# Kernel tuning notes

Hardware: AMD Instinct MI355X
Metric: run time of the kernel (lower is better)

Reference implementation:

```python
import jax, jax.numpy as jnp
import numpy as np

TINY = 1e-9
S, V, H, W = 2, 4, 1024, 1024
PATCH, SKIP = 2, 2
C = PATCH * SKIP
PIX_PER_VIEW = 4096
NP_COARSE = PIX_PER_VIEW // (PATCH * PATCH)   # top-k on coarse grid
N_SAMPLED = NP_COARSE * PATCH * PATCH         # total fine pixels per view
ON_MASK = 0.9
AT_CENTER = 0.8
HC, WC = H // C, W // C


def setup_inputs() -> dict:
    key = jax.random.key(0)
    k1, k2, k3, k4, k5 = jax.random.split(key, 5)
    ys, xs = jnp.meshgrid(jnp.arange(H, dtype=jnp.float32),
                          jnp.arange(W, dtype=jnp.float32), indexing='ij')
    uv1 = jnp.stack([xs.reshape(-1), ys.reshape(-1)])            # (2, H*W): X then Y
    uv = jnp.broadcast_to(uv1[None, None], (S, V, 2, H * W)) + 0.0
    base = jnp.array([[1111.0, 0.0, W / 2.0, 0.0],
                      [0.0, 1111.0, H / 2.0, 0.0],
                      [0.0, 0.0, 1.0, 0.0],
                      [0.0, 0.0, 0.0, 1.0]], dtype=jnp.float32)
    intrinsics = jnp.broadcast_to(base[None], (S, 4, 4)) + 0.0
    A = jax.random.normal(k2, (S, V, 3, 3), dtype=jnp.float32)
    Q, _ = jnp.linalg.qr(A)                                       # random rotations
    t = 2.0 * jax.random.normal(k3, (S, V, 3), dtype=jnp.float32)
    ext = jnp.zeros((S, V, 4, 4), dtype=jnp.float32)
    ext = ext.at[..., :3, :3].set(Q).at[..., :3, 3].set(t).at[..., 3, 3].set(1.0)
    alpha = jax.random.normal(k4, (S, V, H, W), dtype=jnp.float32)
    size = jnp.stack([jnp.full((S, V), H, jnp.int32),
                      jnp.full((S, V), W, jnp.int32)], axis=-1)
    gumbel_u = jax.random.uniform(k5, (S, V, HC * WC), dtype=jnp.float32)
    full_index = jax.random.randint(k1, (S, V), 0, SKIP * SKIP)
    return dict(uv=uv, intrinsics=intrinsics, extrinsics=ext, alpha=alpha,
                size=size, gumbel_u=gumbel_u, full_index=full_index)


def _sample_pixels(uv, alpha, gumbel_u, full_index):
    # mask from alpha, restricted to image center (sampling_at_center=0.8)
    mask = (alpha > 0).astype(jnp.float32)                        # (S,V,H,W)
    r = (1.0 - AT_CENTER) / 2.0
    rh, rw = int(H * r), int(W * r)
    row_ok = (jnp.arange(H) >= rh) & (jnp.arange(H) < H - rh)
    col_ok = (jnp.arange(W) >= rw) & (jnp.arange(W) < W - rw)
    mask = mask * (row_ok[:, None] & col_ok[None, :]).astype(jnp.float32)
    probs = mask / (mask.sum() + 1e-8)                            # global normalization as in torch
    probs = ON_MASK * probs + (1.0 - ON_MASK) / (H * W)
    # pool probabilities onto the coarse (patch*skip) grid
    probs_c = probs.reshape(S, V, HC, C, WC, C).sum(axis=(3, 5))  # (S,V,HC,WC)
    logp = jnp.log(probs_c.reshape(S, V, -1) + TINY)
    g = -jnp.log(-jnp.log(gumbel_u + TINY) + TINY)                # gumbel noise
    idx = jax.lax.top_k(logp + g, NP_COARSE)[1]                   # (S,V,NP_COARSE)
    sm = jnp.zeros((S, V, HC * WC), jnp.float32)
    sm = sm.at[jnp.arange(S)[:, None, None], jnp.arange(V)[None, :, None], idx].set(1.0)
    sm = sm.reshape(S, V, HC, WC)
    # expand each coarse cell into a patch x patch block -> (S,V,H//SKIP,W//SKIP)
    sm = jnp.broadcast_to(sm[:, :, :, None, :, None],
                          (S, V, HC, PATCH, WC, PATCH)).reshape(S, V, H // SKIP, W // SKIP)
    # scatter into a random skip-slot per view, then interleave skip grid
    oh = jax.nn.one_hot(full_index, SKIP * SKIP, dtype=jnp.float32)  # (S,V,SKIP*SKIP)
    full = oh[:, :, :, None, None] * sm[:, :, None, :, :]
    sm = full.reshape(S, V, SKIP, SKIP, H // SKIP, W // SKIP)
    sm = sm.transpose(0, 1, 4, 2, 5, 3).reshape(S, V, H, W)
    # row-major gather of sampled pixels (matches torch boolean-mask gather)
    mflat = sm.reshape(S, V, H * W)
    order = jnp.argsort(-mflat, axis=-1)[..., :N_SAMPLED]         # stable: ones in row-major order
    Xs = jnp.take_along_axis(uv[:, :, 0], order, axis=-1).reshape(S, V, 1, -1, PATCH, PATCH)
    Ys = jnp.take_along_axis(uv[:, :, 1], order, axis=-1).reshape(S, V, 1, -1, PATCH, PATCH)
    return jnp.concatenate([Xs, Ys], axis=2)                      # (S,V,2,NPatch,PATCH,PATCH)


def _rays(uv_s, intrinsics, extrinsics):
    fuv = uv_s.reshape(S, V, 2, -1)                               # (S,V,2,N)
    ray_start = extrinsics[:, :, :3, 3]                           # (S,V,3)
    fx = intrinsics[:, 0, 0][:, None, None]
    fy = intrinsics[:, 1, 1][:, None, None]
    cx = intrinsics[:, 0, 2][:, None, None]
    cy = intrinsics[:, 1, 2][:, None, None]
    x = (fuv[:, :, 0] - cx) / fx                                  # z = 1 lift
    y = (fuv[:, :, 1] - cy) / fy
    ones = jnp.ones_like(x)
    cam = jnp.stack([x, y, ones, ones], axis=2)                   # (S,V,4,N) homogeneous
    world = jnp.einsum('svij,svjn->svin', extrinsics, cam)[:, :, :3]
    d = world - ray_start[..., None]
    d = d / jnp.maximum(jnp.linalg.norm(d, axis=2, keepdims=True), 1e-12)
    return ray_start[:, :, None, :], d.transpose(0, 1, 3, 2)      # (S,V,1,3), (S,V,N,3)


def reference(uv, intrinsics, extrinsics, alpha, size, gumbel_u, full_index):
    uv_s = _sample_pixels(uv, alpha, gumbel_u, full_index)
    ray_start, ray_dir = _rays(uv_s, intrinsics, extrinsics)
    return ray_start, ray_dir, uv_s
```

## Files before the change

kernel.cpp:

```cpp
#include <hip/hip_runtime.h>
#include <math.h>

#define S_ 2
#define V_ 4
#define H_ 1024
#define W_ 1024
#define NCELL 65536
#define NSV 8
#define KSEL 1024
#define CROP_LO 102
#define CROP_HI 922
#define NPIX (H_*W_)

#define NB1 32768
#define NB2 131072
#define NSEG 128
#define HIST_U4 ((NB1 + NB2) * NSV / 4)

#define OFF_SEL   64
#define OFF_SEG   256
#define OFF_CNT   4352
#define OFF_ROW   135424
#define OFF_KEYS  528640
#define OFF_H1    2625792
#define OFF_H2    3674368

static __device__ __forceinline__ unsigned score_key(float score){
  unsigned ub = __float_as_uint(score);
  return (ub & 0x80000000u) ? ~ub : (ub | 0x80000000u);
}

__global__ __launch_bounds__(64) void k_init(unsigned* __restrict__ total){
  if (threadIdx.x == 0) *total = 0u;
}

__global__ __launch_bounds__(256) void k_count(const float* __restrict__ alpha,
                                               unsigned char* __restrict__ cnt,
                                               unsigned* __restrict__ total,
                                               uint4* __restrict__ histz){
  int g = blockIdx.x * 256 + threadIdx.x;
  if (g < HIST_U4) histz[g] = make_uint4(0u, 0u, 0u, 0u);
  int sv = g >> 16;
  int cell = g & (NCELL - 1);
  int hc = cell >> 8;
  int wc = cell & 255;
  const float4* ap = reinterpret_cast<const float4*>(alpha);
  int c = 0;
  int x0 = wc * 4;
#pragma unroll
  for (int dy = 0; dy < 4; ++dy){
    int y = hc * 4 + dy;
    float4 a = ap[(size_t)(sv * H_ + y) * (W_ / 4) + wc];
    if (y >= CROP_LO && y < CROP_HI){
      c += (a.x > 0.0f) & (x0 + 0 >= CROP_LO) & (x0 + 0 < CROP_HI);
      c += (a.y > 0.0f) & (x0 + 1 >= CROP_LO) & (x0 + 1 < CROP_HI);
      c += (a.z > 0.0f) & (x0 + 2 >= CROP_LO) & (x0 + 2 < CROP_HI);
      c += (a.w > 0.0f) & (x0 + 3 >= CROP_LO) & (x0 + 3 < CROP_HI);
    }
  }
  cnt[g] = (unsigned char)c;
  __shared__ unsigned red[256];
  red[threadIdx.x] = (unsigned)c;
  __syncthreads();
  for (int off = 128; off > 0; off >>= 1){
    if (threadIdx.x < off) red[threadIdx.x] += red[threadIdx.x + off];
    __syncthreads();
  }
  if (threadIdx.x == 0) atomicAdd(total, red[0]);
}

__global__ __launch_bounds__(256) void k_scoreh(const unsigned char* __restrict__ cnt,
                                                const float* __restrict__ gum,
                                                const unsigned* __restrict__ total,
                                                unsigned* __restrict__ keys,
                                                unsigned* __restrict__ hist1){
  const int sv = blockIdx.x >> 6;
  const int chunk = blockIdx.x & 63;
  const int t = threadIdx.x;
  __shared__ unsigned h[NB1 / 2];
  for (int i = t; i < NB1 / 2; i += 256) h[i] = 0u;

  const int g0 = sv * NCELL + chunk * 1024 + t * 4;
  const unsigned c4 = *reinterpret_cast<const unsigned*>(cnt + g0);
  const float4 g4 = *reinterpret_cast<const float4*>(gum + g0);

  float T = (float)(*total);
  float denom = __fadd_rn(T, 1e-8f);
  float inv = __fdiv_rn(1.0f, denom);
  const float COFF = (float)((1.0 - 0.9) / (1024.0 * 1024.0));
  float q_on = __fadd_rn(__fmul_rn(0.9f, inv), COFF);

  unsigned kout[4];
  const float gu[4] = {g4.x, g4.y, g4.z, g4.w};
#pragma unroll
  for (int q = 0; q < 4; ++q){
    int k = (int)((c4 >> (8 * q)) & 0xFFu);
    float pc = __fadd_rn(__fmul_rn((float)k, q_on), __fmul_rn((float)(16 - k), COFF));
    float logp = logf(__fadd_rn(pc, 1e-9f));
    float gl = logf(__fadd_rn(gu[q], 1e-9f));
    float gmb = -logf(__fadd_rn(-gl, 1e-9f));
    kout[q] = score_key(__fadd_rn(logp, gmb));
  }
  *reinterpret_cast<uint4*>(keys + g0) = make_uint4(kout[0], kout[1], kout[2], kout[3]);

  __syncthreads();
#pragma unroll
  for (int q = 0; q < 4; ++q){
    unsigned b = kout[q] >> 17;
    atomicAdd(&h[b >> 1], 1u << ((b & 1u) << 4));
  }
  __syncthreads();
  unsigned* hb = hist1 + sv * NB1;
  for (int i = t; i < NB1 / 2; i += 256){
    unsigned w = h[i];
    unsigned lo = w & 0xFFFFu, hi = w >> 16;
    if (lo) atomicAdd(&hb[2 * i + 0], lo);
    if (hi) atomicAdd(&hb[2 * i + 1], hi);
  }
}

__global__ __launch_bounds__(1024) void k_pick1(const unsigned* __restrict__ hist1,
                                                unsigned* __restrict__ sel){
  const int sv = blockIdx.x;
  const int t = threadIdx.x;
  const unsigned* h = hist1 + sv * NB1;
  const unsigned target = KSEL;
  const uint4* h4 = reinterpret_cast<const uint4*>(h + t * 32);
  unsigned csum = 0;
#pragma unroll
  for (int i = 0; i < 8; ++i){
    uint4 v = h4[i];
    csum += v.x + v.y + v.z + v.w;
  }
  __shared__ unsigned sh[1024];
  sh[t] = csum;
  __syncthreads();
  for (int off = 1; off < 1024; off <<= 1){
    unsigned v = (t + off < 1024) ? sh[t + off] : 0u;
    __syncthreads();
    sh[t] += v;
    __syncthreads();
  }
  unsigned sufAbove = sh[t] - csum;
  if (sufAbove < target && sh[t] >= target){
    unsigned cum = sufAbove;
    for (int b = 31; b >= 0; --b){
      unsigned hv = h[t * 32 + b];
      cum += hv;
      if (cum >= target){
        sel[sv * 4 + 0] = (unsigned)(t * 32 + b);
        sel[sv * 4 + 1] = target - (cum - hv);
        break;
      }
    }
  }
}

__global__ __launch_bounds__(256) void k_hist2(const unsigned* __restrict__ keys,
                                               const unsigned* __restrict__ sel,
                                               unsigned* __restrict__ hist2){
  int sv = blockIdx.x >> 5;
  int chunk = blockIdx.x & 31;
  unsigned p15 = sel[sv * 4 + 0];
  const uint4* kp = reinterpret_cast<const uint4*>(keys + sv * NCELL + chunk * 2048);
  unsigned* hb = hist2 + sv * NB2;
#pragma unroll
  for (int i = 0; i < 2; ++i){
    uint4 k4 = kp[threadIdx.x + i * 256];
    if ((k4.x >> 17) == p15) atomicAdd(&hb[k4.x & 0x1FFFFu], 1u);
    if ((k4.y >> 17) == p15) atomicAdd(&hb[k4.y & 0x1FFFFu], 1u);
    if ((k4.z >> 17) == p15) atomicAdd(&hb[k4.z & 0x1FFFFu], 1u);
    if ((k4.w >> 17) == p15) atomicAdd(&hb[k4.w & 0x1FFFFu], 1u);
  }
}

__global__ __launch_bounds__(256) void k_seg2(const unsigned* __restrict__ hist2,
                                              unsigned* __restrict__ segsum){
  int sv = blockIdx.x >> 7;
  int seg = blockIdx.x & (NSEG - 1);
  const uint4* h4 = reinterpret_cast<const uint4*>(hist2 + sv * NB2 + seg * 1024);
  uint4 v = h4[threadIdx.x];
  unsigned csum = v.x + v.y + v.z + v.w;
  __shared__ unsigned red[256];
  red[threadIdx.x] = csum;
  __syncthreads();
  for (int off = 128; off > 0; off >>= 1){
    if (threadIdx.x < off) red[threadIdx.x] += red[threadIdx.x + off];
    __syncthreads();
  }
  if (threadIdx.x == 0) segsum[sv * NSEG + seg] = red[0];
}

__global__ __launch_bounds__(256) void k_pick2c(const unsigned* __restrict__ hist2,
                                                const unsigned* __restrict__ segsum,
                                                unsigned* __restrict__ sel){
  const int sv = blockIdx.x;
  const int t = threadIdx.x;
  __shared__ unsigned ss[NSEG];
  __shared__ int swin;
  __shared__ unsigned stgt;
  if (t < NSEG) ss[t] = segsum[sv * NSEG + t];
  __syncthreads();
  if (t == 0){
    unsigned target = sel[sv * 4 + 1];
    unsigned cum = 0;
    for (int s = NSEG - 1; s >= 0; --s){
      cum += ss[s];
      if (cum >= target){ swin = s; stgt = target - (cum - ss[s]); break; }
    }
  }
  __syncthreads();
  const int s = swin;
  const unsigned t2 = stgt;
  const uint4* h4 = reinterpret_cast<const uint4*>(hist2 + sv * NB2 + s * 1024);
  uint4 v = h4[t];
  unsigned csum = v.x + v.y + v.z + v.w;
  __shared__ unsigned sh[256];
  sh[t] = csum;
  __syncthreads();
  for (int off = 1; off < 256; off <<= 1){
    unsigned y = (t + off < 256) ? sh[t + off] : 0u;
    __syncthreads();
    sh[t] += y;
    __syncthreads();
  }
  unsigned sufAbove = sh[t] - csum;
  if (sufAbove < t2 && sh[t] >= t2){
    unsigned bb[4] = {v.x, v.y, v.z, v.w};
    unsigned cum = sufAbove;
    for (int b = 3; b >= 0; --b){
      cum += bb[b];
      if (cum >= t2){
        sel[sv * 4 + 2] = (sel[sv * 4 + 0] << 17) | (unsigned)(s * 1024 + t * 4 + b);
        sel[sv * 4 + 3] = t2 - (cum - bb[b]);
        break;
      }
    }
  }
}

__global__ __launch_bounds__(256) void k_rowcnt(const unsigned* __restrict__ keys,
                                                const unsigned* __restrict__ sel,
                                                unsigned* __restrict__ rowcnt){
  int gw = blockIdx.x * 4 + (threadIdx.x >> 6);
  int lane = threadIdx.x & 63;
  int sv = gw >> 8;
  int row = gw & 255;
  const unsigned thr = sel[sv * 4 + 2];
  uint4 k4 = *reinterpret_cast<const uint4*>(keys + sv * NCELL + row * 256 + lane * 4);
  unsigned gt = (k4.x > thr) + (k4.y > thr) + (k4.z > thr) + (k4.w > thr);
  unsigned eq = (k4.x == thr) + (k4.y == thr) + (k4.z == thr) + (k4.w == thr);
  unsigned p = (gt << 16) | eq;
#pragma unroll
  for (int off = 1; off < 64; off <<= 1) p += __shfl_xor(p, off, 64);
  if (lane == 0) rowcnt[gw] = p;
}

static __device__ __forceinline__ unsigned block_excl_scan256(unsigned v, unsigned* lds4, int t){
  int lane = t & 63, w = t >> 6;
  unsigned x = v;
#pragma unroll
  for (int off = 1; off < 64; off <<= 1){
    unsigned y = __shfl_up(x, (unsigned)off, 64);
    if (lane >= off) x += y;
  }
  if (lane == 63) lds4[w] = x;
  __syncthreads();
  unsigned base = 0;
  for (int i = 0; i < w; ++i) base += lds4[i];
  __syncthreads();
  return base + x - v;
}

__global__ __launch_bounds__(256) void k_emitray(const unsigned* __restrict__ keys,
                                                 const unsigned* __restrict__ sel,
                                                 const unsigned* __restrict__ rowcnt,
                                                 const int* __restrict__ fidx,
                                                 const float* __restrict__ intr,
                                                 const float* __restrict__ extr,
                                                 float* __restrict__ out){
  const int sv = blockIdx.x >> 6;
  const int t = threadIdx.x;
  __shared__ unsigned lds4[4];
  __shared__ unsigned sM[256], sP[256], sEqb[256];

  const unsigned thr = sel[sv * 4 + 2];
  const unsigned rem = sel[sv * 4 + 3];

  unsigned rc = rowcnt[sv * 256 + t];
  unsigned gt = rc >> 16, eq = rc & 0xFFFFu;
  unsigned eqbase = block_excl_scan256(eq, lds4, t);
  unsigned take_eq = 0;
  if (rem > eqbase){ take_eq = rem - eqbase; if (take_eq > eq) take_eq = eq; }
  unsigned m = gt + take_eq;
  unsigned P = block_excl_scan256(m, lds4, t);
  sM[t] = m; sP[t] = P; sEqb[t] = eqbase;
  __syncthreads();

  const int lane = t & 63;
  const int row = ((blockIdx.x & 63) << 2) + (t >> 6);
  const unsigned rm = sM[row];
  const unsigned rP = sP[row];
  const unsigned reqb = sEqb[row];

  const int s = sv >> 2;
  const float fx = intr[s * 16 + 0];
  const float cx = intr[s * 16 + 2];
  const float fy = intr[s * 16 + 5];
  const float cy = intr[s * 16 + 6];
  const float e00 = extr[sv * 16 + 0], e01 = extr[sv * 16 + 1], e02 = extr[sv * 16 + 2], e03 = extr[sv * 16 + 3];
  const float e10 = extr[sv * 16 + 4], e11 = extr[sv * 16 + 5], e12 = extr[sv * 16 + 6], e13 = extr[sv * 16 + 7];
  const float e20 = extr[sv * 16 + 8], e21 = extr[sv * 16 + 9], e22 = extr[sv * 16 + 10], e23 = extr[sv * 16 + 11];
  if ((blockIdx.x & 63) == 0 && t < 3) out[sv * 3 + t] = extr[sv * 16 + t * 4 + 3];

  const int fi = fidx[sv];
  const int k1 = (fi >> 1) & 1;
  const int k2 = fi & 1;
  float* out_dir = out + S_ * V_ * 3;
  float* out_uvs = out + S_ * V_ * 3 + S_ * V_ * 4096 * 3;

  uint4 k4 = *reinterpret_cast<const uint4*>(keys + sv * NCELL + row * 256 + lane * 4);
  unsigned kk[4] = {k4.x, k4.y, k4.z, k4.w};

  unsigned laneEq = 0;
#pragma unroll
  for (int q = 0; q < 4; ++q) laneEq += (kk[q] == thr);
  unsigned xe = laneEq;
#pragma unroll
  for (int off = 1; off < 64; off <<= 1){
    unsigned y = __shfl_up(xe, (unsigned)off, 64);
    if (lane >= off) xe += y;
  }
  unsigned eqpre = xe - laneEq;

  bool ssel[4];
  unsigned eqr = reqb + eqpre;
  unsigned laneSel = 0;
#pragma unroll
  for (int q = 0; q < 4; ++q){
    bool sq = (kk[q] > thr);
    if (kk[q] == thr){ if (eqr < rem) sq = true; eqr++; }
    ssel[q] = sq;
    laneSel += sq;
  }
  unsigned xs = laneSel;
#pragma unroll
  for (int off = 1; off < 64; off <<= 1){
    unsigned y = __shfl_up(xs, (unsigned)off, 64);
    if (lane >= off) xs += y;
  }
  unsigned jj = xs - laneSel;

  const unsigned baserank = 4u * rP;
#pragma unroll
  for (int q = 0; q < 4; ++q){
    if (!ssel[q]) continue;
    int wc = lane * 4 + q;
    unsigned base = baserank + 2u * jj;
    int y0 = 4 * row + k1;
    int x0 = 4 * wc + k2;
#pragma unroll
    for (int p1 = 0; p1 < 2; ++p1){
#pragma unroll
      for (int p2 = 0; p2 < 2; ++p2){
        unsigned r = base + (unsigned)p1 * 2u * rm + (unsigned)p2;
        float X = (float)(x0 + 2 * p2);
        float Y = (float)(y0 + 2 * p1);
        out_uvs[(sv * 2 + 0) * 4096 + r] = X;
        out_uvs[(sv * 2 + 1) * 4096 + r] = Y;
        float xx = (X - cx) / fx;
        float yy = (Y - cy) / fy;
        float d0 = (e00 * xx + e01 * yy + e02 + e03) - e03;
        float d1 = (e10 * xx + e11 * yy + e12 + e13) - e13;
        float d2 = (e20 * xx + e21 * yy + e22 + e23) - e23;
        float nrm = sqrtf(d0 * d0 + d1 * d1 + d2 * d2);
        float den = fmaxf(nrm, 1e-12f);
        size_t ob = ((size_t)sv * 4096 + r) * 3;
        out_dir[ob + 0] = d0 / den;
        out_dir[ob + 1] = d1 / den;
        out_dir[ob + 2] = d2 / den;
      }
    }
    jj++;
  }
}

extern "C" void kernel_launch(void* const* d_in, const int* in_sizes, int n_in,
                              void* d_out, int out_size, void* d_ws, size_t ws_size,
                              hipStream_t stream){
  (void)in_sizes; (void)n_in; (void)out_size; (void)ws_size;
  const float* intr       = (const float*)d_in[1];
  const float* extr       = (const float*)d_in[2];
  const float* alpha      = (const float*)d_in[3];
  const float* gum        = (const float*)d_in[5];
  const int*   full_index = (const int*)d_in[6];
  float* out = (float*)d_out;

  char* ws = (char*)d_ws;
  unsigned*      total  = (unsigned*)ws;
  unsigned*      sel    = (unsigned*)(ws + OFF_SEL);
  unsigned*      segsum = (unsigned*)(ws + OFF_SEG);
  unsigned char* cnt    = (unsigned char*)(ws + OFF_CNT);
  unsigned*      rowcnt = (unsigned*)(ws + OFF_ROW);
  unsigned*      keys   = (unsigned*)(ws + OFF_KEYS);
  unsigned*      hist1  = (unsigned*)(ws + OFF_H1);
  unsigned*      hist2  = (unsigned*)(ws + OFF_H2);
  uint4*         histz  = (uint4*)(ws + OFF_H1);

  hipLaunchKernelGGL(k_init,    dim3(1), dim3(64), 0, stream, total);
  hipLaunchKernelGGL(k_count,   dim3(NSV * NCELL / 256), dim3(256), 0, stream, alpha, cnt, total, histz);
  hipLaunchKernelGGL(k_scoreh,  dim3(512), dim3(256), 0, stream, cnt, gum, total, keys, hist1);
  hipLaunchKernelGGL(k_pick1,   dim3(NSV), dim3(1024), 0, stream, hist1, sel);
  hipLaunchKernelGGL(k_hist2,   dim3(NSV * 32), dim3(256), 0, stream, keys, sel, hist2);
  hipLaunchKernelGGL(k_seg2,    dim3(NSV * NSEG), dim3(256), 0, stream, hist2, segsum);
  hipLaunchKernelGGL(k_pick2c,  dim3(NSV), dim3(256), 0, stream, hist2, segsum, sel);
  hipLaunchKernelGGL(k_rowcnt,  dim3(512), dim3(256), 0, stream, keys, sel, rowcnt);
  hipLaunchKernelGGL(k_emitray, dim3(512), dim3(256), 0, stream, keys, sel, rowcnt, full_index, intr, extr, out);
}
```

Baseline: 80.19 us.

## Build segment sums inside histogram kernels and pick radix buckets hierarchically

The fused score-plus-histogram kernel is split into a per-cell score kernel and a separate first-level histogram kernel. That histogram kernel also accumulates 128 per-segment sums, so the first pick only needs to scan one 256-bin segment instead of a full 32K-bin prefix scan per view. The second-level histogram kernel now accumulates its segment sums through shared atomics, which removes the separate segment-reduction launch. The segment-sum buffers are zeroed in the init kernel and the cnt buffer shares storage with rowcnt; this is safe because their lifetimes do not overlap, but it adds extra atomics and one more full pass over the keys.

```diff
diff --git a/kernel.cpp b/kernel.cpp
--- a/kernel.cpp
+++ b/kernel.cpp
@@ -10,36 +10,36 @@
 #define KSEL 1024
 #define CROP_LO 102
 #define CROP_HI 922
-#define NPIX (H_*W_)
 
 #define NB1 32768
 #define NB2 131072
-#define NSEG 128
 #define HIST_U4 ((NB1 + NB2) * NSV / 4)
 
 #define OFF_SEL   64
-#define OFF_SEG   256
-#define OFF_CNT   4352
-#define OFF_ROW   135424
-#define OFF_KEYS  528640
-#define OFF_H1    2625792
-#define OFF_H2    3674368
+#define OFF_SEG1  256
+#define OFF_SEG2  4352
+#define OFF_CNT   8448
+#define OFF_ROW   8448
+#define OFF_KEYS  532736
+#define OFF_H1    2629888
+#define OFF_H2    3678464
 
 static __device__ __forceinline__ unsigned score_key(float score){
   unsigned ub = __float_as_uint(score);
   return (ub & 0x80000000u) ? ~ub : (ub | 0x80000000u);
 }
 
-__global__ __launch_bounds__(64) void k_init(unsigned* __restrict__ total){
-  if (threadIdx.x == 0) *total = 0u;
+__global__ __launch_bounds__(1024) void k_init(unsigned* __restrict__ ws32){
+  int t = threadIdx.x;
+  if (t == 0) ws32[0] = 0u;
+  ws32[64 + t] = 0u;
+  ws32[64 + 1024 + t] = 0u;
 }
 
 __global__ __launch_bounds__(256) void k_count(const float* __restrict__ alpha,
                                                unsigned char* __restrict__ cnt,
-                                               unsigned* __restrict__ total,
-                                               uint4* __restrict__ histz){
+                                               unsigned* __restrict__ total){
   int g = blockIdx.x * 256 + threadIdx.x;
-  if (g < HIST_U4) histz[g] = make_uint4(0u, 0u, 0u, 0u);
   int sv = g >> 16;
   int cell = g & (NCELL - 1);
   int hc = cell >> 8;
@@ -69,142 +69,145 @@
   if (threadIdx.x == 0) atomicAdd(total, red[0]);
 }
 
-__global__ __launch_bounds__(256) void k_scoreh(const unsigned char* __restrict__ cnt,
-                                                const float* __restrict__ gum,
-                                                const unsigned* __restrict__ total,
-                                                unsigned* __restrict__ keys,
-                                                unsigned* __restrict__ hist1){
-  const int sv = blockIdx.x >> 6;
-  const int chunk = blockIdx.x & 63;
-  const int t = threadIdx.x;
-  __shared__ unsigned h[NB1 / 2];
-  for (int i = t; i < NB1 / 2; i += 256) h[i] = 0u;
-
-  const int g0 = sv * NCELL + chunk * 1024 + t * 4;
-  const unsigned c4 = *reinterpret_cast<const unsigned*>(cnt + g0);
-  const float4 g4 = *reinterpret_cast<const float4*>(gum + g0);
-
+__global__ __launch_bounds__(256) void k_score(const unsigned char* __restrict__ cnt,
+                                               const float* __restrict__ gum,
+                                               const unsigned* __restrict__ total,
+                                               unsigned* __restrict__ keys,
+                                               uint4* __restrict__ histz){
+  int g = blockIdx.x * 256 + threadIdx.x;
+  if (g < HIST_U4) histz[g] = make_uint4(0u, 0u, 0u, 0u);
   float T = (float)(*total);
   float denom = __fadd_rn(T, 1e-8f);
   float inv = __fdiv_rn(1.0f, denom);
   const float COFF = (float)((1.0 - 0.9) / (1024.0 * 1024.0));
   float q_on = __fadd_rn(__fmul_rn(0.9f, inv), COFF);
-
-  unsigned kout[4];
-  const float gu[4] = {g4.x, g4.y, g4.z, g4.w};
-#pragma unroll
-  for (int q = 0; q < 4; ++q){
-    int k = (int)((c4 >> (8 * q)) & 0xFFu);
-    float pc = __fadd_rn(__fmul_rn((float)k, q_on), __fmul_rn((float)(16 - k), COFF));
-    float logp = logf(__fadd_rn(pc, 1e-9f));
-    float gl = logf(__fadd_rn(gu[q], 1e-9f));
-    float gmb = -logf(__fadd_rn(-gl, 1e-9f));
-    kout[q] = score_key(__fadd_rn(logp, gmb));
-  }
-  *reinterpret_cast<uint4*>(keys + g0) = make_uint4(kout[0], kout[1], kout[2], kout[3]);
-
-  __syncthreads();
-#pragma unroll
-  for (int q = 0; q < 4; ++q){
-    unsigned b = kout[q] >> 17;
-    atomicAdd(&h[b >> 1], 1u << ((b & 1u) << 4));
+  int k = cnt[g];
+  float pc = __fadd_rn(__fmul_rn((float)k, q_on), __fmul_rn((float)(16 - k), COFF));
+  float logp = logf(__fadd_rn(pc, 1e-9f));
+  float u = gum[g];
+  float gl = logf(__fadd_rn(u, 1e-9f));
+  float gmb = -logf(__fadd_rn(-gl, 1e-9f));
+  keys[g] = score_key(__fadd_rn(logp, gmb));
+}
+
+__global__ __launch_bounds__(256) void k_hist1(const unsigned* __restrict__ keys,
+                                               unsigned* __restrict__ hist1,
+                                               unsigned* __restrict__ segsum1){
+  int sv = blockIdx.x >> 5;
+  int chunk = blockIdx.x & 31;
+  __shared__ unsigned h[NB1 / 2];
+  for (int i = threadIdx.x; i < NB1 / 2; i += 256) h[i] = 0u;
+  __syncthreads();
+  const uint4* kp = reinterpret_cast<const uint4*>(keys + sv * NCELL + chunk * 2048);
+#pragma unroll
+  for (int i = 0; i < 2; ++i){
+    uint4 k4 = kp[threadIdx.x + i * 256];
+    unsigned b;
+    b = k4.x >> 17; atomicAdd(&h[b >> 1], 1u << ((b & 1u) << 4));
+    b = k4.y >> 17; atomicAdd(&h[b >> 1], 1u << ((b & 1u) << 4));
+    b = k4.z >> 17; atomicAdd(&h[b >> 1], 1u << ((b & 1u) << 4));
+    b = k4.w >> 17; atomicAdd(&h[b >> 1], 1u << ((b & 1u) << 4));
   }
   __syncthreads();
   unsigned* hb = hist1 + sv * NB1;
-  for (int i = t; i < NB1 / 2; i += 256){
+  for (int i = threadIdx.x; i < NB1 / 2; i += 256){
     unsigned w = h[i];
     unsigned lo = w & 0xFFFFu, hi = w >> 16;
     if (lo) atomicAdd(&hb[2 * i + 0], lo);
     if (hi) atomicAdd(&hb[2 * i + 1], hi);
   }
-}
-
-__global__ __launch_bounds__(1024) void k_pick1(const unsigned* __restrict__ hist1,
+  if (threadIdx.x < 128){
+    unsigned s = 0;
+    for (int i = 0; i < 128; ++i){
+      unsigned w = h[threadIdx.x * 128 + i];
+      s += (w & 0xFFFFu) + (w >> 16);
+    }
+    if (s) atomicAdd(&segsum1[sv * 128 + threadIdx.x], s);
+  }
+}
+
+__global__ __launch_bounds__(256) void k_pick1b(const unsigned* __restrict__ hist1,
+                                                const unsigned* __restrict__ segsum1,
                                                 unsigned* __restrict__ sel){
   const int sv = blockIdx.x;
   const int t = threadIdx.x;
-  const unsigned* h = hist1 + sv * NB1;
-  const unsigned target = KSEL;
-  const uint4* h4 = reinterpret_cast<const uint4*>(h + t * 32);
-  unsigned csum = 0;
-#pragma unroll
-  for (int i = 0; i < 8; ++i){
-    uint4 v = h4[i];
-    csum += v.x + v.y + v.z + v.w;
-  }
-  __shared__ unsigned sh[1024];
-  sh[t] = csum;
-  __syncthreads();
-  for (int off = 1; off < 1024; off <<= 1){
-    unsigned v = (t + off < 1024) ? sh[t + off] : 0u;
+  __shared__ unsigned ss[128];
+  __shared__ int swin;
+  __shared__ unsigned stgt;
+  __shared__ unsigned sh[256];
+  if (t < 128) ss[t] = segsum1[sv * 128 + t];
+  __syncthreads();
+  if (t == 0){
+    unsigned target = KSEL, cum = 0;
+    for (int s = 127; s >= 0; --s){
+      cum += ss[s];
+      if (cum >= target){ swin = s; stgt = target - (cum - ss[s]); break; }
+    }
+  }
+  __syncthreads();
+  unsigned v = hist1[sv * NB1 + swin * 256 + t];
+  sh[t] = v;
+  __syncthreads();
+  for (int off = 1; off < 256; off <<= 1){
+    unsigned y = (t + off < 256) ? sh[t + off] : 0u;
     __syncthreads();
-    sh[t] += v;
+    sh[t] += y;
     __syncthreads();
   }
-  unsigned sufAbove = sh[t] - csum;
-  if (sufAbove < target && sh[t] >= target){
-    unsigned cum = sufAbove;
-    for (int b = 31; b >= 0; --b){
-      unsigned hv = h[t * 32 + b];
-      cum += hv;
-      if (cum >= target){
-        sel[sv * 4 + 0] = (unsigned)(t * 32 + b);
-        sel[sv * 4 + 1] = target - (cum - hv);
-        break;
-      }
-    }
+  unsigned sufAbove = sh[t] - v;
+  if (sufAbove < stgt && sh[t] >= stgt){
+    sel[sv * 4 + 0] = (unsigned)(swin * 256 + t);
+    sel[sv * 4 + 1] = stgt - sufAbove;
   }
 }
 
 __global__ __launch_bounds__(256) void k_hist2(const unsigned* __restrict__ keys,
                                                const unsigned* __restrict__ sel,
-                                               unsigned* __restrict__ hist2){
+                                               unsigned* __restrict__ hist2,
+                                               unsigned* __restrict__ segsum2){
   int sv = blockIdx.x >> 5;
   int chunk = blockIdx.x & 31;
   unsigned p15 = sel[sv * 4 + 0];
+  __shared__ unsigned seg[128];
+  if (threadIdx.x < 128) seg[threadIdx.x] = 0u;
+  __syncthreads();
   const uint4* kp = reinterpret_cast<const uint4*>(keys + sv * NCELL + chunk * 2048);
   unsigned* hb = hist2 + sv * NB2;
 #pragma unroll
   for (int i = 0; i < 2; ++i){
     uint4 k4 = kp[threadIdx.x + i * 256];
-    if ((k4.x >> 17) == p15) atomicAdd(&hb[k4.x & 0x1FFFFu], 1u);
-    if ((k4.y >> 17) == p15) atomicAdd(&hb[k4.y & 0x1FFFFu], 1u);
-    if ((k4.z >> 17) == p15) atomicAdd(&hb[k4.z & 0x1FFFFu], 1u);
-    if ((k4.w >> 17) == p15) atomicAdd(&hb[k4.w & 0x1FFFFu], 1u);
-  }
-}
-
-__global__ __launch_bounds__(256) void k_seg2(const unsigned* __restrict__ hist2,
-                                              unsigned* __restrict__ segsum){
-  int sv = blockIdx.x >> 7;
-  int seg = blockIdx.x & (NSEG - 1);
-  const uint4* h4 = reinterpret_cast<const uint4*>(hist2 + sv * NB2 + seg * 1024);
-  uint4 v = h4[threadIdx.x];
-  unsigned csum = v.x + v.y + v.z + v.w;
-  __shared__ unsigned red[256];
-  red[threadIdx.x] = csum;
-  __syncthreads();
-  for (int off = 128; off > 0; off >>= 1){
-    if (threadIdx.x < off) red[threadIdx.x] += red[threadIdx.x + off];
-    __syncthreads();
-  }
-  if (threadIdx.x == 0) segsum[sv * NSEG + seg] = red[0];
+    unsigned kk[4] = {k4.x, k4.y, k4.z, k4.w};
+#pragma unroll
+    for (int q = 0; q < 4; ++q){
+      if ((kk[q] >> 17) == p15){
+        unsigned low = kk[q] & 0x1FFFFu;
+        atomicAdd(&hb[low], 1u);
+        atomicAdd(&seg[low >> 10], 1u);
+      }
+    }
+  }
+  __syncthreads();
+  if (threadIdx.x < 128){
+    unsigned s = seg[threadIdx.x];
+    if (s) atomicAdd(&segsum2[sv * 128 + threadIdx.x], s);
+  }
 }
 
 __global__ __launch_bounds__(256) void k_pick2c(const unsigned* __restrict__ hist2,
-                                                const unsigned* __restrict__ segsum,
+                                                const unsigned* __restrict__ segsum2,
                                                 unsigned* __restrict__ sel){
   const int sv = blockIdx.x;
   const int t = threadIdx.x;
-  __shared__ unsigned ss[NSEG];
+  __shared__ unsigned ss[128];
   __shared__ int swin;
   __shared__ unsigned stgt;
-  if (t < NSEG) ss[t] = segsum[sv * NSEG + t];
+  __shared__ unsigned sh[256];
+  if (t < 128) ss[t] = segsum2[sv * 128 + t];
   __syncthreads();
   if (t == 0){
     unsigned target = sel[sv * 4 + 1];
     unsigned cum = 0;
-    for (int s = NSEG - 1; s >= 0; --s){
+    for (int s = 127; s >= 0; --s){
       cum += ss[s];
       if (cum >= target){ swin = s; stgt = target - (cum - ss[s]); break; }
     }
@@ -212,10 +215,8 @@
   __syncthreads();
   const int s = swin;
   const unsigned t2 = stgt;
-  const uint4* h4 = reinterpret_cast<const uint4*>(hist2 + sv * NB2 + s * 1024);
-  uint4 v = h4[t];
+  uint4 v = reinterpret_cast<const uint4*>(hist2 + sv * NB2 + s * 1024)[t];
   unsigned csum = v.x + v.y + v.z + v.w;
-  __shared__ unsigned sh[256];
   sh[t] = csum;
   __syncthreads();
   for (int off = 1; off < 256; off <<= 1){
@@ -397,23 +398,25 @@
   float* out = (float*)d_out;
 
   char* ws = (char*)d_ws;
-  unsigned*      total  = (unsigned*)ws;
-  unsigned*      sel    = (unsigned*)(ws + OFF_SEL);
-  unsigned*      segsum = (unsigned*)(ws + OFF_SEG);
-  unsigned char* cnt    = (unsigned char*)(ws + OFF_CNT);
-  unsigned*      rowcnt = (unsigned*)(ws + OFF_ROW);
-  unsigned*      keys   = (unsigned*)(ws + OFF_KEYS);
-  unsigned*      hist1  = (unsigned*)(ws + OFF_H1);
-  unsigned*      hist2  = (unsigned*)(ws + OFF_H2);
-  uint4*         histz  = (uint4*)(ws + OFF_H1);
-
-  hipLaunchKernelGGL(k_init,    dim3(1), dim3(64), 0, stream, total);
-  hipLaunchKernelGGL(k_count,   dim3(NSV * NCELL / 256), dim3(256), 0, stream, alpha, cnt, total, histz);
-  hipLaunchKernelGGL(k_scoreh,  dim3(512), dim3(256), 0, stream, cnt, gum, total, keys, hist1);
-  hipLaunchKernelGGL(k_pick1,   dim3(NSV), dim3(1024), 0, stream, hist1, sel);
-  hipLaunchKernelGGL(k_hist2,   dim3(NSV * 32), dim3(256), 0, stream, keys, sel, hist2);
-  hipLaunchKernelGGL(k_seg2,    dim3(NSV * NSEG), dim3(256), 0, stream, hist2, segsum);
-  hipLaunchKernelGGL(k_pick2c,  dim3(NSV), dim3(256), 0, stream, hist2, segsum, sel);
+  unsigned*      ws32    = (unsigned*)ws;
+  unsigned*      total   = (unsigned*)ws;
+  unsigned*      sel     = (unsigned*)(ws + OFF_SEL);
+  unsigned*      segsum1 = (unsigned*)(ws + OFF_SEG1);
+  unsigned*      segsum2 = (unsigned*)(ws + OFF_SEG2);
+  unsigned char* cnt     = (unsigned char*)(ws + OFF_CNT);
+  unsigned*      rowcnt  = (unsigned*)(ws + OFF_ROW);
+  unsigned*      keys    = (unsigned*)(ws + OFF_KEYS);
+  unsigned*      hist1   = (unsigned*)(ws + OFF_H1);
+  unsigned*      hist2   = (unsigned*)(ws + OFF_H2);
+  uint4*         histz   = (uint4*)(ws + OFF_H1);
+
+  hipLaunchKernelGGL(k_init,    dim3(1), dim3(1024), 0, stream, ws32);
+  hipLaunchKernelGGL(k_count,   dim3(NSV * NCELL / 256), dim3(256), 0, stream, alpha, cnt, total);
+  hipLaunchKernelGGL(k_score,   dim3(NSV * NCELL / 256), dim3(256), 0, stream, cnt, gum, total, keys, histz);
+  hipLaunchKernelGGL(k_hist1,   dim3(NSV * 32), dim3(256), 0, stream, keys, hist1, segsum1);
+  hipLaunchKernelGGL(k_pick1b,  dim3(NSV), dim3(256), 0, stream, hist1, segsum1, sel);
+  hipLaunchKernelGGL(k_hist2,   dim3(NSV * 32), dim3(256), 0, stream, keys, sel, hist2, segsum2);
+  hipLaunchKernelGGL(k_pick2c,  dim3(NSV), dim3(256), 0, stream, hist2, segsum2, sel);
   hipLaunchKernelGGL(k_rowcnt,  dim3(512), dim3(256), 0, stream, keys, sel, rowcnt);
   hipLaunchKernelGGL(k_emitray, dim3(512), dim3(256), 0, stream, keys, sel, rowcnt, full_index, intr, extr, out);
 }
```

Measured after the change: 82.48 us. 1.03x slower.
